# Kernel tuning notes

Measured on AMD Instinct MI355X. Metric: run time of the kernel, lower is better.

## Reference

```python
import jax, jax.numpy as jnp
import numpy as np

D_MODEL = 1024
NUM_HEADS = 16
HEAD_DIM = D_MODEL // NUM_HEADS


def setup_inputs() -> dict:
    key = jax.random.key(0)
    kx, kq, kk, kv, ko = jax.random.split(key, 5)
    B, S = 4, 2048
    scale = 1.0 / np.sqrt(D_MODEL)
    return {
        "x": jax.random.normal(kx, (B, S, D_MODEL), dtype=jnp.float32),
        # bias-free linear weights, torch convention [out, in]
        "wq": jax.random.normal(kq, (D_MODEL, D_MODEL), dtype=jnp.float32) * scale,
        "wk": jax.random.normal(kk, (D_MODEL, D_MODEL), dtype=jnp.float32) * scale,
        "wv": jax.random.normal(kv, (D_MODEL, D_MODEL), dtype=jnp.float32) * scale,
        "wo": jax.random.normal(ko, (D_MODEL, D_MODEL), dtype=jnp.float32) * scale,
    }


def reference(x, wq, wk, wv, wo):
    B, S, D = x.shape
    H, Hd = NUM_HEADS, HEAD_DIM
    # projections (y = x @ W^T), reshape to [B, H, S, Hd]
    def proj(w):
        return jnp.einsum('bsd,ed->bse', x, w).reshape(B, S, H, Hd).transpose(0, 2, 1, 3)
    q, k, v = proj(wq), proj(wk), proj(wv)
    # scaled dot-product attention with causal mask
    scores = jnp.einsum('bhqd,bhkd->bhqk', q, k) / jnp.sqrt(jnp.asarray(Hd, x.dtype))
    causal = jnp.tril(jnp.ones((S, S), dtype=bool))  # [S, S]
    scores = jnp.where(causal[None, None], scores, jnp.asarray(-jnp.inf, x.dtype))
    attn = jax.nn.softmax(scores, axis=-1)
    out = jnp.einsum('bhqk,bhkd->bhqd', attn, v)  # [B, H, S, Hd]
    out = out.transpose(0, 2, 1, 3).reshape(B, S, D)
    return jnp.einsum('bsd,ed->bse', out, wo)
```

## Files before the change

### kernel.cpp

```cpp
#include <hip/hip_runtime.h>
#include <hip/hip_bf16.h>
#include <math.h>


#define S_LEN 2048
#define DM    1024
#define NH    16
#define HD    64
#define M_ROWS 8192

typedef __attribute__((ext_vector_type(8))) short bf16x8;
typedef __attribute__((ext_vector_type(4))) float f32x4;
typedef __attribute__((ext_vector_type(16))) float f32x16;

__device__ __forceinline__ float bf2f(unsigned short u) {
  union { unsigned int i; float f; } c; c.i = ((unsigned int)u) << 16; return c.f;
}
__device__ __forceinline__ unsigned short f2bf(float f) {
  unsigned int x = __float_as_uint(f);
  if ((x & 0x7fffffffu) > 0x7f800000u) return (unsigned short)0x7fc0u;
  return (unsigned short)((x + 0x7fffu + ((x >> 16) & 1u)) >> 16);
}
__device__ __forceinline__ void gl_lds16(const unsigned short* g, unsigned short* l) {
  __builtin_amdgcn_global_load_lds(
      (const __attribute__((address_space(1))) unsigned int*)g,
      (__attribute__((address_space(3))) unsigned int*)l, 16, 0, 0);
}

#define FENCE() asm volatile("" ::: "memory")

__global__ __launch_bounds__(256) void cvt_bf16(const float* __restrict__ in,
                                                unsigned short* __restrict__ out) {
  const int i = blockIdx.x * 256 + threadIdx.x;
  float4 a = ((const float4*)in)[2 * i];
  float4 b = ((const float4*)in)[2 * i + 1];
  ushort4 r0, r1;
  r0.x = f2bf(a.x); r0.y = f2bf(a.y); r0.z = f2bf(a.z); r0.w = f2bf(a.w);
  r1.x = f2bf(b.x); r1.y = f2bf(b.y); r1.z = f2bf(b.z); r1.w = f2bf(b.w);
  ((ushort4*)out)[2 * i] = r0;
  ((ushort4*)out)[2 * i + 1] = r1;
}

__global__ __launch_bounds__(256) void cvt_w3(const float* __restrict__ w0,
                                              const float* __restrict__ w1,
                                              const float* __restrict__ w2,
                                              unsigned short* __restrict__ out) {
  const int idx = blockIdx.x;
  const int which = idx >> 9;
  const float* src = (which == 0) ? w0 : (which == 1) ? w1 : w2;
  unsigned short* dst = out + (size_t)which * (DM * DM);
  const int i = (idx & 511) * 256 + threadIdx.x;
  float4 a = ((const float4*)src)[2 * i];
  float4 b = ((const float4*)src)[2 * i + 1];
  ushort4 r0, r1;
  r0.x = f2bf(a.x); r0.y = f2bf(a.y); r0.z = f2bf(a.z); r0.w = f2bf(a.w);
  r1.x = f2bf(b.x); r1.y = f2bf(b.y); r1.z = f2bf(b.z); r1.w = f2bf(b.w);
  ((ushort4*)dst)[2 * i] = r0;
  ((ushort4*)dst)[2 * i + 1] = r1;
}

template <int OUT_MODE>
__global__ __launch_bounds__(512, 4) void gemm_bt(const unsigned short* __restrict__ A,
                                                  const unsigned short* __restrict__ Wall,
                                                  unsigned short* __restrict__ outB,
                                                  float* __restrict__ outF) {
  __shared__ __align__(16) unsigned short As[3 * 8192];
  __shared__ __align__(16) unsigned short Bs[3 * 4096];
  const int m0 = blockIdx.x * 256;
  const int n0 = blockIdx.y * 128;
  const int tid = threadIdx.x;
  const int lane = tid & 63, w = tid >> 6;
  const int quad = lane >> 4, l15 = lane & 15;
  const int wrow = w >> 1, wcol = w & 1;

  const int skg = w & 3, srq = w >> 2;
  const unsigned short* agA = A    + (size_t)(m0 + srq * 64 + lane) * DM + skg * 8;
  const unsigned short* bgB = Wall + (size_t)(n0 + srq * 64 + lane) * DM + skg * 8;
  const int lA0 = skg * 2048 + srq * 512;
  const int lA1 = lA0 + 1024;
  const int lB  = skg * 1024 + srq * 512;
  const int raA = quad * 2048 + (wrow * 64 + l15) * 8;
  const int raB = quad * 1024 + (wcol * 64 + l15) * 8;

  f32x4 acc[4][4];
#pragma unroll
  for (int i = 0; i < 4; ++i)
#pragma unroll
    for (int j = 0; j < 4; ++j) { acc[i][j].x = 0.f; acc[i][j].y = 0.f; acc[i][j].z = 0.f; acc[i][j].w = 0.f; }

#define STAGE3(T, SB) do {                                                   \
    const unsigned short* ap_ = agA + (size_t)(T) * 32;                      \
    gl_lds16(ap_,          &As[(SB) * 8192 + lA0]);                          \
    gl_lds16(ap_ + 131072, &As[(SB) * 8192 + lA1]);                          \
    gl_lds16(bgB + (size_t)(T) * 32, &Bs[(SB) * 4096 + lB]);                 \
  } while (0)

#define COMPUTE(CB) do {                                                     \
    bf16x8 af_[4], bq_[4];                                                   \
    _Pragma("unroll")                                                        \
    for (int mi = 0; mi < 4; ++mi)                                           \
      af_[mi] = *(const bf16x8*)&As[(CB) * 8192 + raA + mi * 128];           \
    _Pragma("unroll")                                                        \
    for (int ni = 0; ni < 4; ++ni)                                           \
      bq_[ni] = *(const bf16x8*)&Bs[(CB) * 4096 + raB + ni * 128];           \
    __builtin_amdgcn_s_setprio(1);                                           \
    _Pragma("unroll")                                                        \
    for (int mi = 0; mi < 4; ++mi)                                           \
      _Pragma("unroll")                                                      \
      for (int ni = 0; ni < 4; ++ni)                                         \
        acc[mi][ni] = __builtin_amdgcn_mfma_f32_16x16x32_bf16(af_[mi], bq_[ni], acc[mi][ni], 0, 0, 0); \
    __builtin_amdgcn_s_setprio(0);                                           \
  } while (0)

#define SUBSTEP(T, SB, CB) do {                                              \
    asm volatile("s_waitcnt vmcnt(3)" ::: "memory");                         \
    __builtin_amdgcn_s_barrier();                                            \
    FENCE();                                                                 \
    STAGE3((T), (SB));                                                       \
    COMPUTE(CB);                                                             \
    FENCE();                                                                 \
  } while (0)

  STAGE3(0, 0);
  STAGE3(1, 1);

  for (int t = 0; t < 30; t += 3) {
    SUBSTEP(t + 2, 2, 0);
    SUBSTEP(t + 3, 0, 1);
    SUBSTEP(t + 4, 1, 2);
  }
  asm volatile("s_waitcnt vmcnt(3)" ::: "memory");
  __builtin_amdgcn_s_barrier();
  FENCE();
  COMPUTE(0);
  asm volatile("s_waitcnt vmcnt(0)" ::: "memory");
  __builtin_amdgcn_s_barrier();
  FENCE();
  COMPUTE(1);

#undef SUBSTEP
#undef COMPUTE
#undef STAGE3

  const float oscale = (OUT_MODE == 0 && n0 < 1024) ? 0.125f : 1.0f;
#pragma unroll
  for (int mi = 0; mi < 4; ++mi) {
#pragma unroll
    for (int reg = 0; reg < 4; ++reg) {
      const int m = m0 + wrow * 64 + mi * 16 + quad * 4 + reg;
#pragma unroll
      for (int ni = 0; ni < 4; ++ni) {
        const int e = n0 + wcol * 64 + ni * 16 + l15;
        const float v = acc[mi][ni][reg];
        if (OUT_MODE == 0) {
          const int z = e >> 10;
          const int e10 = e & 1023;
          const int b = m >> 11, s = m & (S_LEN - 1);
          const int h = e10 >> 6, hd = e10 & 63;
          outB[(size_t)z * (M_ROWS * DM) +
               (((size_t)(b * NH + h)) * S_LEN + s) * HD + hd] = f2bf(v * oscale);
        } else {
          outF[(size_t)m * DM + e] = v;
        }
      }
    }
  }
}

__global__ __launch_bounds__(256, 4) void attn_mfma(const unsigned short* __restrict__ Q,
                                                    const unsigned short* __restrict__ K,
                                                    const unsigned short* __restrict__ V,
                                                    unsigned short* __restrict__ O) {
  __shared__ unsigned short Ks[64][72];
  __shared__ unsigned short Vt[64][72];
  const int bh = blockIdx.x;
  const int bx = 15 - (int)blockIdx.y;
  const int tid = threadIdx.x;
  const int w = tid >> 6, lane = tid & 63;
  const int l31 = lane & 31, hi = lane >> 5;
  const size_t base = (size_t)bh * S_LEN * HD;
  const int b = bh >> 4, h = bh & 15;
  const int wq0 = bx * 128 + w * 32;
  const int diag_jt = 2 * bx + (w >> 1);
  const int jt_blk = 2 * bx + 1;
  const int kr0 = tid >> 3, kc0 = (tid & 7) * 8;
  const int vs = (tid & 31) * 2, vh = (tid >> 5) * 8;

  bf16x8 qb[4];
#pragma unroll
  for (int ds = 0; ds < 4; ++ds)
    qb[ds] = *(const bf16x8*)(Q + base + (size_t)(wq0 + l31) * HD + ds * 16 + hi * 8);

  f32x16 o0, o1;
#pragma unroll
  for (int r = 0; r < 16; ++r) { o0[r] = 0.f; o1[r] = 0.f; }
  float l_acc = 0.f;

  for (int jt = 0; jt <= jt_blk; ++jt) {
    __syncthreads();
    {
      const unsigned short* kgp = K + base + (size_t)jt * 64 * HD;
      const unsigned short* vgp = V + base + (size_t)jt * 64 * HD;
      *(uint4*)&Ks[kr0][kc0]      = *(const uint4*)(kgp + kr0 * HD + kc0);
      *(uint4*)&Ks[kr0 + 32][kc0] = *(const uint4*)(kgp + (kr0 + 32) * HD + kc0);
      uint4 r0 = *(const uint4*)(vgp + (size_t)vs * HD + vh);
      uint4 r1 = *(const uint4*)(vgp + (size_t)(vs + 1) * HD + vh);
      const unsigned int* a0 = (const unsigned int*)&r0;
      const unsigned int* a1 = (const unsigned int*)&r1;
#pragma unroll
      for (int j = 0; j < 4; ++j) {
        *(unsigned int*)&Vt[vh + 2 * j][vs]     = __builtin_amdgcn_perm(a1[j], a0[j], 0x05040100u);
        *(unsigned int*)&Vt[vh + 2 * j + 1][vs] = __builtin_amdgcn_perm(a1[j], a0[j], 0x07060302u);
      }
    }
    __syncthreads();

    if (jt <= diag_jt) {
      const bool diag = (jt == diag_jt);
      for (int kb = 0; kb < 2; ++kb) {
        const bool kb_zero = diag && ((w & 1) == 0) && (kb == 1);
        const bool kb_part = diag && (kb == (w & 1));
        if (kb_zero) continue;

        f32x16 sa;
#pragma unroll
        for (int r = 0; r < 16; ++r) sa[r] = 0.f;
        __builtin_amdgcn_s_setprio(1);
#pragma unroll
        for (int ds = 0; ds < 4; ++ds) {
          bf16x8 kf = *(const bf16x8*)&Ks[kb * 32 + l31][ds * 16 + hi * 8];
          sa = __builtin_amdgcn_mfma_f32_32x32x16_bf16(kf, qb[ds], sa, 0, 0, 0);
        }
        __builtin_amdgcn_s_setprio(0);

        float p[16];
        if (kb_part) {
#pragma unroll
          for (int r = 0; r < 16; ++r) {
            const int krel = (r & 3) + 8 * (r >> 2) + 4 * hi;
            p[r] = __expf((l31 >= krel) ? sa[r] : -1.0e30f);
          }
        } else {
#pragma unroll
          for (int r = 0; r < 16; ++r) p[r] = __expf(sa[r]);
        }
        l_acc += (((p[0] + p[1]) + (p[2] + p[3])) + ((p[4] + p[5]) + (p[6] + p[7])))
               + (((p[8] + p[9]) + (p[10] + p[11])) + ((p[12] + p[13]) + (p[14] + p[15])));

        unsigned int pk[8], sk[8];
#pragma unroll
        for (int g = 0; g < 4; ++g) {
          pk[2 * g]     = __builtin_amdgcn_perm(__float_as_uint(p[4 * g + 1]), __float_as_uint(p[4 * g]),     0x07060302u);
          pk[2 * g + 1] = __builtin_amdgcn_perm(__float_as_uint(p[4 * g + 3]), __float_as_uint(p[4 * g + 2]), 0x07060302u);
        }
#pragma unroll
        for (int i = 0; i < 8; ++i) sk[i] = (unsigned int)__shfl_xor((int)pk[i], 32);

#pragma unroll
        for (int sl = 0; sl < 2; ++sl) {
          const int g0 = 2 * sl, g1 = 2 * sl + 1;
          union { unsigned int u[4]; bf16x8 v; } fa;
          fa.u[0] = hi ? sk[2 * g1]     : pk[2 * g0];
          fa.u[1] = hi ? sk[2 * g1 + 1] : pk[2 * g0 + 1];
          fa.u[2] = hi ? pk[2 * g1]     : sk[2 * g0];
          fa.u[3] = hi ? pk[2 * g1 + 1] : sk[2 * g0 + 1];
          const int s = kb * 2 + sl;
          bf16x8 v0 = *(const bf16x8*)&Vt[l31][s * 16 + hi * 8];
          bf16x8 v1 = *(const bf16x8*)&Vt[32 + l31][s * 16 + hi * 8];
          __builtin_amdgcn_s_setprio(1);
          o0 = __builtin_amdgcn_mfma_f32_32x32x16_bf16(fa.v, v0, o0, 0, 0, 0);
          o1 = __builtin_amdgcn_mfma_f32_32x32x16_bf16(fa.v, v1, o1, 0, 0, 0);
          __builtin_amdgcn_s_setprio(0);
        }
      }
    }
  }

  const float lf = l_acc + __shfl_xor(l_acc, 32);
  const float inv = 1.0f / lf;
#pragma unroll
  for (int r = 0; r < 16; ++r) {
    const int qrel = (r & 3) + 8 * (r >> 2) + 4 * hi;
    const float invr = __shfl(inv, qrel);
    const size_t orow = (size_t)(b * S_LEN + wq0 + qrel) * DM + h * HD;
    O[orow + l31]      = f2bf(o0[r] * invr);
    O[orow + 32 + l31] = f2bf(o1[r] * invr);
  }
}

extern "C" void kernel_launch(void* const* d_in, const int* in_sizes, int n_in,
                              void* d_out, int out_size, void* d_ws, size_t ws_size,
                              hipStream_t stream) {
  const float* x  = (const float*)d_in[0];
  const float* wq = (const float*)d_in[1];
  const float* wk = (const float*)d_in[2];
  const float* wv = (const float*)d_in[3];
  const float* wo = (const float*)d_in[4];

  unsigned short* Qb = (unsigned short*)d_ws;
  unsigned short* Kb = Qb + (size_t)M_ROWS * DM;
  unsigned short* Vb = Kb + (size_t)M_ROWS * DM;
  unsigned short* Xb = Vb + (size_t)M_ROWS * DM;
  unsigned short* Ob = Xb;
  (void)Kb; (void)Vb;

  unsigned short* Wstash = (unsigned short*)d_out;

  dim3 bb(256);
  dim3 gb(512);

  hipLaunchKernelGGL(cvt_bf16, dim3((M_ROWS * DM) / 2048), bb, 0, stream, x, Xb);
  hipLaunchKernelGGL(cvt_w3, dim3(3 * (DM * DM) / 2048), bb, 0, stream, wq, wk, wv, Wstash);
  hipLaunchKernelGGL((gemm_bt<0>), dim3(M_ROWS / 256, 3 * DM / 128), gb, 0, stream,
                     Xb, Wstash, Qb, (float*)nullptr);
  hipLaunchKernelGGL(attn_mfma, dim3(64, 16), bb, 0, stream, Qb, Qb + (size_t)M_ROWS * DM,
                     Qb + 2 * (size_t)M_ROWS * DM, Ob);
  hipLaunchKernelGGL(cvt_bf16, dim3((DM * DM) / 2048), bb, 0, stream, wo, Qb);
  hipLaunchKernelGGL((gemm_bt<1>), dim3(M_ROWS / 256, DM / 128), gb, 0, stream,
                     Ob, Qb, (unsigned short*)nullptr, (float*)d_out);
}
```

Before: 200.0 us.

## Halve GEMM workgroup to 4 waves, each computing a 128x64 tile

The projection GEMMs now launch 256-thread workgroups instead of 512, keeping the same 256x128 block tile. Each wave computes 128x64 outputs with 8x4 accumulators and issues six global-to-LDS loads per k-step instead of three, so the vmcnt waits change to match. This raises the MFMA work per LDS fragment load and reduces barrier participants, at the cost of more accumulator registers and fewer waves to hide latency.

```diff
diff --git a/kernel.cpp b/kernel.cpp
--- a/kernel.cpp
+++ b/kernel.cpp
@@ -60,7 +60,7 @@
 }
 
 template <int OUT_MODE>
-__global__ __launch_bounds__(512, 4) void gemm_bt(const unsigned short* __restrict__ A,
+__global__ __launch_bounds__(256, 2) void gemm_bt(const unsigned short* __restrict__ A,
                                                   const unsigned short* __restrict__ Wall,
                                                   unsigned short* __restrict__ outB,
                                                   float* __restrict__ outF) {
@@ -73,39 +73,41 @@
   const int quad = lane >> 4, l15 = lane & 15;
   const int wrow = w >> 1, wcol = w & 1;
 
-  const int skg = w & 3, srq = w >> 2;
-  const unsigned short* agA = A    + (size_t)(m0 + srq * 64 + lane) * DM + skg * 8;
-  const unsigned short* bgB = Wall + (size_t)(n0 + srq * 64 + lane) * DM + skg * 8;
-  const int lA0 = skg * 2048 + srq * 512;
-  const int lA1 = lA0 + 1024;
-  const int lB  = skg * 1024 + srq * 512;
-  const int raA = quad * 2048 + (wrow * 64 + l15) * 8;
+  const unsigned short* agA = A    + (size_t)(m0 + lane) * DM + w * 8;
+  const unsigned short* bgB = Wall + (size_t)(n0 + lane) * DM + w * 8;
+  const int lA0 = w * 2048;
+  const int lB0 = w * 1024;
+  const int raA = quad * 2048 + (wrow * 128 + l15) * 8;
   const int raB = quad * 1024 + (wcol * 64 + l15) * 8;
 
-  f32x4 acc[4][4];
-#pragma unroll
-  for (int i = 0; i < 4; ++i)
+  f32x4 acc[8][4];
+#pragma unroll
+  for (int i = 0; i < 8; ++i)
 #pragma unroll
     for (int j = 0; j < 4; ++j) { acc[i][j].x = 0.f; acc[i][j].y = 0.f; acc[i][j].z = 0.f; acc[i][j].w = 0.f; }
 
-#define STAGE3(T, SB) do {                                                   \
+#define STAGE6(T, SB) do {                                                   \
     const unsigned short* ap_ = agA + (size_t)(T) * 32;                      \
-    gl_lds16(ap_,          &As[(SB) * 8192 + lA0]);                          \
-    gl_lds16(ap_ + 131072, &As[(SB) * 8192 + lA1]);                          \
-    gl_lds16(bgB + (size_t)(T) * 32, &Bs[(SB) * 4096 + lB]);                 \
+    const unsigned short* bp_ = bgB + (size_t)(T) * 32;                      \
+    gl_lds16(ap_,               &As[(SB) * 8192 + lA0]);                     \
+    gl_lds16(ap_ + 64 * DM,     &As[(SB) * 8192 + lA0 + 512]);               \
+    gl_lds16(ap_ + 128 * DM,    &As[(SB) * 8192 + lA0 + 1024]);              \
+    gl_lds16(ap_ + 192 * DM,    &As[(SB) * 8192 + lA0 + 1536]);              \
+    gl_lds16(bp_,               &Bs[(SB) * 4096 + lB0]);                     \
+    gl_lds16(bp_ + 64 * DM,     &Bs[(SB) * 4096 + lB0 + 512]);               \
   } while (0)
 
 #define COMPUTE(CB) do {                                                     \
-    bf16x8 af_[4], bq_[4];                                                   \
+    bf16x8 af_[8], bq_[4];                                                   \
     _Pragma("unroll")                                                        \
-    for (int mi = 0; mi < 4; ++mi)                                           \
+    for (int mi = 0; mi < 8; ++mi)                                           \
       af_[mi] = *(const bf16x8*)&As[(CB) * 8192 + raA + mi * 128];           \
     _Pragma("unroll")                                                        \
     for (int ni = 0; ni < 4; ++ni)                                           \
       bq_[ni] = *(const bf16x8*)&Bs[(CB) * 4096 + raB + ni * 128];           \
     __builtin_amdgcn_s_setprio(1);                                           \
     _Pragma("unroll")                                                        \
-    for (int mi = 0; mi < 4; ++mi)                                           \
+    for (int mi = 0; mi < 8; ++mi)                                           \
       _Pragma("unroll")                                                      \
       for (int ni = 0; ni < 4; ++ni)                                         \
         acc[mi][ni] = __builtin_amdgcn_mfma_f32_16x16x32_bf16(af_[mi], bq_[ni], acc[mi][ni], 0, 0, 0); \
@@ -113,23 +115,23 @@
   } while (0)
 
 #define SUBSTEP(T, SB, CB) do {                                              \
-    asm volatile("s_waitcnt vmcnt(3)" ::: "memory");                         \
+    asm volatile("s_waitcnt vmcnt(6)" ::: "memory");                         \
     __builtin_amdgcn_s_barrier();                                            \
     FENCE();                                                                 \
-    STAGE3((T), (SB));                                                       \
+    STAGE6((T), (SB));                                                       \
     COMPUTE(CB);                                                             \
     FENCE();                                                                 \
   } while (0)
 
-  STAGE3(0, 0);
-  STAGE3(1, 1);
+  STAGE6(0, 0);
+  STAGE6(1, 1);
 
   for (int t = 0; t < 30; t += 3) {
     SUBSTEP(t + 2, 2, 0);
     SUBSTEP(t + 3, 0, 1);
     SUBSTEP(t + 4, 1, 2);
   }
-  asm volatile("s_waitcnt vmcnt(3)" ::: "memory");
+  asm volatile("s_waitcnt vmcnt(6)" ::: "memory");
   __builtin_amdgcn_s_barrier();
   FENCE();
   COMPUTE(0);
@@ -140,14 +142,14 @@
 
 #undef SUBSTEP
 #undef COMPUTE
-#undef STAGE3
+#undef STAGE6
 
   const float oscale = (OUT_MODE == 0 && n0 < 1024) ? 0.125f : 1.0f;
 #pragma unroll
-  for (int mi = 0; mi < 4; ++mi) {
+  for (int mi = 0; mi < 8; ++mi) {
 #pragma unroll
     for (int reg = 0; reg < 4; ++reg) {
-      const int m = m0 + wrow * 64 + mi * 16 + quad * 4 + reg;
+      const int m = m0 + wrow * 128 + mi * 16 + quad * 4 + reg;
 #pragma unroll
       for (int ni = 0; ni < 4; ++ni) {
         const int e = n0 + wcol * 64 + ni * 16 + l15;
@@ -307,15 +309,14 @@
   unsigned short* Wstash = (unsigned short*)d_out;
 
   dim3 bb(256);
-  dim3 gb(512);
 
   hipLaunchKernelGGL(cvt_bf16, dim3((M_ROWS * DM) / 2048), bb, 0, stream, x, Xb);
   hipLaunchKernelGGL(cvt_w3, dim3(3 * (DM * DM) / 2048), bb, 0, stream, wq, wk, wv, Wstash);
-  hipLaunchKernelGGL((gemm_bt<0>), dim3(M_ROWS / 256, 3 * DM / 128), gb, 0, stream,
+  hipLaunchKernelGGL((gemm_bt<0>), dim3(M_ROWS / 256, 3 * DM / 128), bb, 0, stream,
                      Xb, Wstash, Qb, (float*)nullptr);
   hipLaunchKernelGGL(attn_mfma, dim3(64, 16), bb, 0, stream, Qb, Qb + (size_t)M_ROWS * DM,
                      Qb + 2 * (size_t)M_ROWS * DM, Ob);
   hipLaunchKernelGGL(cvt_bf16, dim3((DM * DM) / 2048), bb, 0, stream, wo, Qb);
-  hipLaunchKernelGGL((gemm_bt<1>), dim3(M_ROWS / 256, DM / 128), gb, 0, stream,
+  hipLaunchKernelGGL((gemm_bt<1>), dim3(M_ROWS / 256, DM / 128), bb, 0, stream,
                      Ob, Qb, (unsigned short*)nullptr, (float*)d_out);
 }
```

Measured after the change: 215.6 us. +7.8%, slower.

## Load GEMM A-operand fragments directly from global into registers, bypassing LDS

Applied to the files above, without the earlier changes.

The GEMM no longer stages the A tile in shared memory. Each wave loads its A fragments straight from global memory into double-buffered registers, one k-step ahead, while B keeps its triple-buffered LDS staging. This removes LDS traffic and capacity for A and may raise occupancy. In exchange, each A row is fetched once per wave column instead of once per block, so global/L2 traffic for A doubles, and the direct loads can stall the MFMA loop. The wait counts are tightened to match the new pipeline.

```diff
diff --git a/kernel.cpp b/kernel.cpp
--- a/kernel.cpp
+++ b/kernel.cpp
@@ -64,23 +64,18 @@
                                                   const unsigned short* __restrict__ Wall,
                                                   unsigned short* __restrict__ outB,
                                                   float* __restrict__ outF) {
-  __shared__ __align__(16) unsigned short As[3 * 8192];
   __shared__ __align__(16) unsigned short Bs[3 * 4096];
   const int m0 = blockIdx.x * 256;
   const int n0 = blockIdx.y * 128;
   const int tid = threadIdx.x;
   const int lane = tid & 63, w = tid >> 6;
   const int quad = lane >> 4, l15 = lane & 15;
-  const int wrow = w >> 1, wcol = w & 1;
-
-  const int skg = w & 3, srq = w >> 2;
-  const unsigned short* agA = A    + (size_t)(m0 + srq * 64 + lane) * DM + skg * 8;
-  const unsigned short* bgB = Wall + (size_t)(n0 + srq * 64 + lane) * DM + skg * 8;
-  const int lA0 = skg * 2048 + srq * 512;
-  const int lA1 = lA0 + 1024;
-  const int lB  = skg * 1024 + srq * 512;
-  const int raA = quad * 2048 + (wrow * 64 + l15) * 8;
-  const int raB = quad * 1024 + (wcol * 64 + l15) * 8;
+  const int wr = w >> 1, wc = w & 1;
+
+  const unsigned short* agA = A + (size_t)(m0 + wr * 64 + l15) * DM + quad * 8;
+  const unsigned short* bgB = Wall + (size_t)(n0 + (w & 1) * 64 + lane) * DM + (w >> 1) * 8;
+  const int sB  = (w >> 1) * 1024 + (w & 1) * 512;
+  const int raB = quad * 1024 + (wc * 64 + l15) * 8;
 
   f32x4 acc[4][4];
 #pragma unroll
@@ -88,69 +83,89 @@
 #pragma unroll
     for (int j = 0; j < 4; ++j) { acc[i][j].x = 0.f; acc[i][j].y = 0.f; acc[i][j].z = 0.f; acc[i][j].w = 0.f; }
 
-#define STAGE3(T, SB) do {                                                   \
-    const unsigned short* ap_ = agA + (size_t)(T) * 32;                      \
-    gl_lds16(ap_,          &As[(SB) * 8192 + lA0]);                          \
-    gl_lds16(ap_ + 131072, &As[(SB) * 8192 + lA1]);                          \
-    gl_lds16(bgB + (size_t)(T) * 32, &Bs[(SB) * 4096 + lB]);                 \
+  bf16x8 aA[4], aB[4];
+
+#define LDA_INTO(DST_, T_) do {                                              \
+    DST_[0] = *(const bf16x8*)(agA + (size_t)(T_) * 32);                     \
+    DST_[1] = *(const bf16x8*)(agA + (size_t)(T_) * 32 + 16 * DM);           \
+    DST_[2] = *(const bf16x8*)(agA + (size_t)(T_) * 32 + 32 * DM);           \
+    DST_[3] = *(const bf16x8*)(agA + (size_t)(T_) * 32 + 48 * DM);           \
   } while (0)
 
-#define COMPUTE(CB) do {                                                     \
-    bf16x8 af_[4], bq_[4];                                                   \
-    _Pragma("unroll")                                                        \
-    for (int mi = 0; mi < 4; ++mi)                                           \
-      af_[mi] = *(const bf16x8*)&As[(CB) * 8192 + raA + mi * 128];           \
+#define STB(T_, S_) gl_lds16(bgB + (size_t)(T_) * 32, &Bs[(S_) * 4096 + sB])
+
+#define CMP(SRC_, CB_) do {                                                  \
+    bf16x8 bq_[4];                                                           \
     _Pragma("unroll")                                                        \
     for (int ni = 0; ni < 4; ++ni)                                           \
-      bq_[ni] = *(const bf16x8*)&Bs[(CB) * 4096 + raB + ni * 128];           \
+      bq_[ni] = *(const bf16x8*)&Bs[(CB_) * 4096 + raB + ni * 128];          \
     __builtin_amdgcn_s_setprio(1);                                           \
     _Pragma("unroll")                                                        \
     for (int mi = 0; mi < 4; ++mi)                                           \
       _Pragma("unroll")                                                      \
       for (int ni = 0; ni < 4; ++ni)                                         \
-        acc[mi][ni] = __builtin_amdgcn_mfma_f32_16x16x32_bf16(af_[mi], bq_[ni], acc[mi][ni], 0, 0, 0); \
+        acc[mi][ni] = __builtin_amdgcn_mfma_f32_16x16x32_bf16(SRC_[mi], bq_[ni], acc[mi][ni], 0, 0, 0); \
     __builtin_amdgcn_s_setprio(0);                                           \
   } while (0)
 
-#define SUBSTEP(T, SB, CB) do {                                              \
-    asm volatile("s_waitcnt vmcnt(3)" ::: "memory");                         \
+#define VM1 asm volatile("s_waitcnt vmcnt(1)" ::: "memory")
+#define VM0 asm volatile("s_waitcnt vmcnt(0)" ::: "memory")
+
+#define ITER(T_, CUR_, NXT_, CB_, SB_) do {                                  \
+    VM1;                                                                     \
     __builtin_amdgcn_s_barrier();                                            \
     FENCE();                                                                 \
-    STAGE3((T), (SB));                                                       \
-    COMPUTE(CB);                                                             \
+    LDA_INTO(NXT_, (T_) + 1);                                                \
+    FENCE();                                                                 \
+    STB((T_) + 2, SB_);                                                      \
+    FENCE();                                                                 \
+    CMP(CUR_, CB_);                                                          \
     FENCE();                                                                 \
   } while (0)
 
-  STAGE3(0, 0);
-  STAGE3(1, 1);
-
-  for (int t = 0; t < 30; t += 3) {
-    SUBSTEP(t + 2, 2, 0);
-    SUBSTEP(t + 3, 0, 1);
-    SUBSTEP(t + 4, 1, 2);
+  STB(0, 0);
+  FENCE();
+  LDA_INTO(aA, 0);
+  FENCE();
+  STB(1, 1);
+  FENCE();
+
+  for (int t = 0; t < 30; t += 6) {
+    ITER(t,     aA, aB, 0, 2);
+    ITER(t + 1, aB, aA, 1, 0);
+    ITER(t + 2, aA, aB, 2, 1);
+    ITER(t + 3, aB, aA, 0, 2);
+    ITER(t + 4, aA, aB, 1, 0);
+    ITER(t + 5, aB, aA, 2, 1);
   }
-  asm volatile("s_waitcnt vmcnt(3)" ::: "memory");
+  VM1;
   __builtin_amdgcn_s_barrier();
   FENCE();
-  COMPUTE(0);
-  asm volatile("s_waitcnt vmcnt(0)" ::: "memory");
+  LDA_INTO(aB, 31);
+  FENCE();
+  CMP(aA, 0);
+  FENCE();
+  VM0;
   __builtin_amdgcn_s_barrier();
   FENCE();
-  COMPUTE(1);
-
-#undef SUBSTEP
-#undef COMPUTE
-#undef STAGE3
+  CMP(aB, 1);
+
+#undef ITER
+#undef VM0
+#undef VM1
+#undef CMP
+#undef STB
+#undef LDA_INTO
 
   const float oscale = (OUT_MODE == 0 && n0 < 1024) ? 0.125f : 1.0f;
 #pragma unroll
   for (int mi = 0; mi < 4; ++mi) {
 #pragma unroll
     for (int reg = 0; reg < 4; ++reg) {
-      const int m = m0 + wrow * 64 + mi * 16 + quad * 4 + reg;
+      const int m = m0 + wr * 64 + mi * 16 + quad * 4 + reg;
 #pragma unroll
       for (int ni = 0; ni < 4; ++ni) {
-        const int e = n0 + wcol * 64 + ni * 16 + l15;
+        const int e = n0 + wc * 64 + ni * 16 + l15;
         const float v = acc[mi][ni][reg];
         if (OUT_MODE == 0) {
           const int z = e >> 10;
```

After: 258.1 us. 29.0% more time.
